# Kernel optimization log

Measured on AMD Instinct MI355X. Metric: run time of the kernel, lower is better.

## Reference

```python
import jax, jax.numpy as jnp
import numpy as np

B, D, V, T = 256, 1024, 32000, 64  # num_seqs, hidden dim, vocab, history len


def setup_inputs() -> dict:
    key = jax.random.key(0)
    ks = jax.random.split(key, 8)
    hidden = jax.random.normal(ks[0], (B, D), dtype=jnp.float32)
    embedding = jax.random.normal(ks[1], (V, D), dtype=jnp.float32) * (1.0 / np.sqrt(D))
    output_tokens = jax.random.randint(ks[2], (B, T), 0, V, dtype=jnp.int64)
    presence_penalties = jax.random.uniform(ks[3], (B,), dtype=jnp.float32)
    frequency_penalties = jax.random.uniform(ks[4], (B,), dtype=jnp.float32)
    temperatures = jax.random.uniform(ks[5], (B,), dtype=jnp.float32) + 0.5  # > eps
    top_ps = jax.random.uniform(ks[6], (B,), dtype=jnp.float32) * 0.5 + 0.5  # in [0.5, 1.0)
    top_ks = jax.random.randint(ks[7], (B,), 1, V, dtype=jnp.int64)
    return {
        "hidden": hidden,
        "embedding": embedding,
        "output_tokens": output_tokens,
        "presence_penalties": presence_penalties,
        "frequency_penalties": frequency_penalties,
        "temperatures": temperatures,
        "top_ps": top_ps,
        "top_ks": top_ks,
    }


def reference(hidden, embedding, output_tokens, presence_penalties,
              frequency_penalties, temperatures, top_ps, top_ks):
    # 1) logits = pruned hidden states @ embedding^T  -> [B, V]
    logits = jnp.einsum("bd,vd->bv", hidden, embedding)
    b, v = logits.shape

    # 2) presence/frequency penalties via per-row token histogram (np.bincount equiv)
    rows = jnp.broadcast_to(jnp.arange(b)[:, None], output_tokens.shape)
    counts = jnp.zeros((b, v), logits.dtype).at[rows, output_tokens].add(1.0)
    logits = logits - frequency_penalties[:, None] * counts \
                    - presence_penalties[:, None] * (counts > 0).astype(logits.dtype)

    # 3) temperature scaling
    logits = logits / temperatures[:, None]

    # 4) probabilities
    probs = jax.nn.softmax(logits, axis=-1)

    # 5) top-p / top-k: descending sort, cumsum masks, scatter back via inverse perm
    order = jnp.argsort(-probs, axis=-1)                       # descending order
    probs_sort = jnp.take_along_axis(probs, order, axis=-1)
    probs_cum = jnp.cumsum(probs_sort, axis=-1)
    top_p_mask = (probs_cum - probs_sort) > top_ps[:, None]
    top_k_mask = jnp.arange(v)[None, :] >= top_ks[:, None]
    probs_sort = jnp.where(top_p_mask | top_k_mask, 0.0, probs_sort)
    inv = jnp.argsort(order, axis=-1)
    filtered_probs = jnp.take_along_axis(probs_sort, inv, axis=-1)  # original order
    return filtered_probs
```

## Files before the change

### kernel.cpp

```cpp
#include <hip/hip_runtime.h>
#include <math.h>

#define NB 256
#define NV 32000
#define ND 1024
#define NT 64

#define GN 64
#define ASTR 40
#define NKB 64
#define ASLAB (256 * ASTR)
#define NGBLK (NV / GN)
#define INV2048F 4.8828125e-4f

#define NBIN 1024
#define HSTR 1032
#define HTOT (4 * HSTR)
#define FIX2 4294967296.0
#define SMASK ((1ull << 48) - 1ull)
#define SMEM_BYTES (NV * 4 + HTOT * 4)

typedef _Float16 f16x8 __attribute__((ext_vector_type(8)));
typedef _Float16 f16x4 __attribute__((ext_vector_type(4)));
typedef float f32x16 __attribute__((ext_vector_type(16)));
typedef __attribute__((address_space(3))) void lds_void;
typedef __attribute__((address_space(1))) void glb_void;

struct RowP2 {
  unsigned long long basePack;
  unsigned long long toppZfix;
  unsigned pfx;
  int ktop;
  float invZ;
  unsigned ustar;
  int m;
  int cEq;
};

__device__ __forceinline__ unsigned mono_enc(float f) {
  unsigned u = __float_as_uint(f);
  return (u & 0x80000000u) ? ~u : (u | 0x80000000u);
}
__device__ __forceinline__ float mono_dec(unsigned u) {
  return (u & 0x80000000u) ? __uint_as_float(u & 0x7FFFFFFFu) : __uint_as_float(~u);
}

__global__ __launch_bounds__(256) void convert_A(const float* __restrict__ hidden,
                                                 _Float16* __restrict__ A3) {
  const int g = blockIdx.x * 256 + threadIdx.x;
  const int kb = g >> 10, rc = g & 1023, r = rc >> 2, c = rc & 3;
  const float4 a4 = *(const float4*)(hidden + (size_t)r * ND + kb * 16 + c * 4);
  const float v[4] = {a4.x, a4.y, a4.z, a4.w};
  f16x4 h4, q4;
#pragma unroll
  for (int q = 0; q < 4; q++) {
    const _Float16 h = (_Float16)v[q];
    h4[q] = h;
    q4[q] = (_Float16)((v[q] - (float)h) * 2048.0f);
  }
  _Float16* base = A3 + (size_t)kb * ASLAB + r * ASTR;
  *(f16x4*)(base + c * 4) = h4;
  *(f16x4*)(base + 16 + c * 4) = q4;
}

__global__ __launch_bounds__(256, 2) void gemm_f16s(
    const float* __restrict__ Bm, const _Float16* __restrict__ A3,
    const float* __restrict__ temp, unsigned* __restrict__ rowmax,
    float* __restrict__ C) {
  __shared__ _Float16 Als[2][ASLAB];
  __shared__ _Float16 Bls[2][GN * ASTR];
  __shared__ float s_invT[256];
  __shared__ unsigned s_pm[256];

  const int t = threadIdx.x;
  const int l = t & 63, w = t >> 6;
  const int n0 = blockIdx.x * GN;
  s_invT[t] = 1.0f / temp[t];
  s_pm[t] = 0u;

  f32x16 accH[2][2] = {};
  f32x16 accC[2][2] = {};

  const int bn = t >> 2, bk4 = (t & 3) * 4;
  const int l31 = l & 31, lh = l >> 5;
  const int ka = lh * 8;
  const int mb = w * 64;

  const float* browp = Bm + (size_t)(n0 + bn) * ND + bk4;
  const char* gaBase = (const char*)A3 + w * 5120 + l * 16;
  char* laB0 = (char*)&Als[0][0] + w * 5120;
  char* laB1 = (char*)&Als[1][0] + w * 5120;

#define ISSUE_A(kbn, LA)                                                        \
  do {                                                                          \
    const char* ga_ = gaBase + (size_t)(kbn) * (ASLAB * 2);                     \
    _Pragma("unroll") for (int i_ = 0; i_ < 5; i_++)                            \
        __builtin_amdgcn_global_load_lds((const glb_void*)(ga_ + i_ * 1024),    \
                                         (lds_void*)((LA) + i_ * 1024), 16, 0,  \
                                         0);                                    \
  } while (0)

#define BCONV(BV, DST)                                                          \
  do {                                                                          \
    f16x4 h4_, q4_;                                                             \
    const float vv_[4] = {(BV).x, (BV).y, (BV).z, (BV).w};                      \
    _Pragma("unroll") for (int j_ = 0; j_ < 4; j_++) {                          \
      const _Float16 h_ = (_Float16)vv_[j_];                                    \
      h4_[j_] = h_;                                                             \
      q4_[j_] = (_Float16)((vv_[j_] - (float)h_) * 2048.0f);                    \
    }                                                                           \
    _Float16* prow_ = (DST) + bn * ASTR;                                        \
    *(f16x4*)(prow_ + bk4) = h4_;                                               \
    *(f16x4*)(prow_ + 16 + bk4) = q4_;                                          \
  } while (0)

#define COMPUTE(CUR)                                                                       \
  do {                                                                                     \
    const _Float16* Ap_ = &Als[CUR][0] + (size_t)(mb + l31) * ASTR + ka;                   \
    const _Float16* Bp_ = &Bls[CUR][0] + (size_t)l31 * ASTR + ka;                          \
    f16x8 a0h_ = *(const f16x8*)(Ap_);                                                     \
    f16x8 a1h_ = *(const f16x8*)(Ap_ + 32 * ASTR);                                         \
    f16x8 b0h_ = *(const f16x8*)(Bp_);                                                     \
    f16x8 b1h_ = *(const f16x8*)(Bp_ + 32 * ASTR);                                         \
    accH[0][0] = __builtin_amdgcn_mfma_f32_32x32x16_f16(a0h_, b0h_, accH[0][0], 0, 0, 0);  \
    accH[0][1] = __builtin_amdgcn_mfma_f32_32x32x16_f16(a0h_, b1h_, accH[0][1], 0, 0, 0);  \
    accH[1][0] = __builtin_amdgcn_mfma_f32_32x32x16_f16(a1h_, b0h_, accH[1][0], 0, 0, 0);  \
    accH[1][1] = __builtin_amdgcn_mfma_f32_32x32x16_f16(a1h_, b1h_, accH[1][1], 0, 0, 0);  \
    f16x8 b0q_ = *(const f16x8*)(Bp_ + 16);                                                \
    f16x8 b1q_ = *(const f16x8*)(Bp_ + 32 * ASTR + 16);                                    \
    accC[0][0] = __builtin_amdgcn_mfma_f32_32x32x16_f16(a0h_, b0q_, accC[0][0], 0, 0, 0);  \
    accC[0][1] = __builtin_amdgcn_mfma_f32_32x32x16_f16(a0h_, b1q_, accC[0][1], 0, 0, 0);  \
    accC[1][0] = __builtin_amdgcn_mfma_f32_32x32x16_f16(a1h_, b0q_, accC[1][0], 0, 0, 0);  \
    accC[1][1] = __builtin_amdgcn_mfma_f32_32x32x16_f16(a1h_, b1q_, accC[1][1], 0, 0, 0);  \
    f16x8 a0q_ = *(const f16x8*)(Ap_ + 16);                                                \
    f16x8 a1q_ = *(const f16x8*)(Ap_ + 32 * ASTR + 16);                                    \
    accC[0][0] = __builtin_amdgcn_mfma_f32_32x32x16_f16(a0q_, b0h_, accC[0][0], 0, 0, 0);  \
    accC[0][1] = __builtin_amdgcn_mfma_f32_32x32x16_f16(a0q_, b1h_, accC[0][1], 0, 0, 0);  \
    accC[1][0] = __builtin_amdgcn_mfma_f32_32x32x16_f16(a1q_, b0h_, accC[1][0], 0, 0, 0);  \
    accC[1][1] = __builtin_amdgcn_mfma_f32_32x32x16_f16(a1q_, b1h_, accC[1][1], 0, 0, 0);  \
  } while (0)

  ISSUE_A(0, laB0);
  __builtin_amdgcn_sched_barrier(0);
  float4 bv0 = *(const float4*)(browp);
  __builtin_amdgcn_sched_barrier(0);
  float4 bvA = *(const float4*)(browp + 16);
  __builtin_amdgcn_sched_barrier(0);
  asm volatile("s_waitcnt vmcnt(1)" ::: "memory");
  BCONV(bv0, &Bls[0][0]);
  asm volatile("s_waitcnt lgkmcnt(0)\ns_barrier" ::: "memory");

  float4 bvB;
  for (int kb = 0; kb < 62; kb += 2) {
    ISSUE_A(kb + 1, laB1);
    __builtin_amdgcn_sched_barrier(0);
    bvB = *(const float4*)(browp + (size_t)(kb + 2) * 16);
    __builtin_amdgcn_sched_barrier(0);
    asm volatile("s_waitcnt vmcnt(7)" ::: "memory");
    COMPUTE(0);
    __builtin_amdgcn_sched_barrier(0);
    asm volatile("s_waitcnt vmcnt(6)" ::: "memory");
    BCONV(bvA, &Bls[1][0]);
    asm volatile("s_waitcnt lgkmcnt(0)\ns_barrier" ::: "memory");

    ISSUE_A(kb + 2, laB0);
    __builtin_amdgcn_sched_barrier(0);
    bvA = *(const float4*)(browp + (size_t)(kb + 3) * 16);
    __builtin_amdgcn_sched_barrier(0);
    asm volatile("s_waitcnt vmcnt(7)" ::: "memory");
    COMPUTE(1);
    __builtin_amdgcn_sched_barrier(0);
    asm volatile("s_waitcnt vmcnt(6)" ::: "memory");
    BCONV(bvB, &Bls[0][0]);
    asm volatile("s_waitcnt lgkmcnt(0)\ns_barrier" ::: "memory");
  }

  ISSUE_A(63, laB1);
  __builtin_amdgcn_sched_barrier(0);
  asm volatile("s_waitcnt vmcnt(6)" ::: "memory");
  COMPUTE(0);
  __builtin_amdgcn_sched_barrier(0);
  asm volatile("s_waitcnt vmcnt(5)" ::: "memory");
  BCONV(bvA, &Bls[1][0]);
  asm volatile("s_waitcnt lgkmcnt(0)\ns_barrier" ::: "memory");

  asm volatile("s_waitcnt vmcnt(0)" ::: "memory");
  COMPUTE(1);

#undef ISSUE_A
#undef BCONV
#undef COMPUTE

#pragma unroll
  for (int mi = 0; mi < 2; mi++) {
#pragma unroll
    for (int r = 0; r < 16; r++) {
      const int row = mb + mi * 32 + (r & 3) + 8 * (r >> 2) + 4 * lh;
      const float it = s_invT[row];
      float v0 = (accH[mi][0][r] + accC[mi][0][r] * INV2048F) * it;
      float v1 = (accH[mi][1][r] + accC[mi][1][r] * INV2048F) * it;
      C[(size_t)row * NV + n0 + l31] = v0;
      C[(size_t)row * NV + n0 + 32 + l31] = v1;
      float mx = fmaxf(v0, v1);
#pragma unroll
      for (int o = 1; o < 32; o <<= 1) mx = fmaxf(mx, __shfl_xor(mx, o));
      if (l31 == 0) atomicMax(&s_pm[row], mono_enc(mx));
    }
  }
  __syncthreads();
  atomicMax(&rowmax[t], s_pm[t]);
}

__global__ __launch_bounds__(1024) void sample_row(
    float* __restrict__ buf, const unsigned* __restrict__ rowmax,
    const int* __restrict__ toks, const float* __restrict__ pres,
    const float* __restrict__ freq, const float* __restrict__ temp,
    const float* __restrict__ topp_a, const int* __restrict__ topk_a) {
  extern __shared__ char smem[];
  float* e = (float*)smem;
  unsigned* hist = (unsigned*)(smem + NV * 4);
  unsigned long long* suf = (unsigned long long*)hist;
  __shared__ int s_tok[NT];
  __shared__ int s_bs;
  __shared__ RowP2 sp;

  const int b = blockIdx.x, t = threadIdx.x;
  const int cp = (t >> 6) & 1;
  unsigned* loP = hist + cp * HSTR;
  unsigned* hcP = hist + 2 * HSTR + cp * HSTR;
  float* row = buf + (size_t)b * NV;

#define HACC(EV, BIN)                                                    \
  do {                                                                   \
    unsigned long long f_ = (unsigned long long)((double)(EV) * FIX2);   \
    unsigned flo_ = (unsigned)f_;                                        \
    unsigned old_ = atomicAdd(&loP[BIN], flo_);                          \
    unsigned hc_ = 0x10000u + (unsigned)(f_ >> 32) +                     \
                   ((old_ + flo_ < flo_) ? 1u : 0u);                     \
    atomicAdd(&hcP[BIN], hc_);                                           \
  } while (0)

  if (t < NT) s_tok[t] = toks[b * NT + t];
  for (int i = t; i < HTOT; i += 1024) hist[i] = 0u;
  for (int i4 = t; i4 < NV / 4; i4 += 1024)
    *(float4*)(e + i4 * 4) = *(const float4*)(row + i4 * 4);
  __syncthreads();

  if (t < NT) {
    const int tk = s_tok[t];
    bool first = true; int cnt = 0;
    for (int j = 0; j < NT; j++)
      if (s_tok[j] == tk) { if (j < t) first = false; cnt++; }
    if (first) e[tk] -= (freq[b] * (float)cnt + pres[b]) / temp[b];
  }
  __syncthreads();

  const float M = mono_dec(rowmax[b]);
  for (int i4 = t; i4 < NV / 4; i4 += 1024) {
    float4 x4 = *(const float4*)(e + i4 * 4);
    float4 e4;
    e4.x = expf(x4.x - M); e4.y = expf(x4.y - M);
    e4.z = expf(x4.z - M); e4.w = expf(x4.w - M);
    *(float4*)(e + i4 * 4) = e4;
    unsigned k;
    k = __float_as_uint(e4.x); if (k) HACC(e4.x, k >> 20);
    k = __float_as_uint(e4.y); if (k) HACC(e4.y, k >> 20);
    k = __float_as_uint(e4.z); if (k) HACC(e4.z, k >> 20);
    k = __float_as_uint(e4.w); if (k) HACC(e4.w, k >> 20);
  }
  __syncthreads();

  for (int level = 0; level < 3; level++) {
    const unsigned lo0 = hist[t], lo1 = hist[HSTR + t];
    const unsigned hc0 = hist[2 * HSTR + t], hc1 = hist[3 * HSTR + t];
    const unsigned c = (hc0 >> 16) + (hc1 >> 16);
    const unsigned long long sum =
        (((unsigned long long)((hc0 & 0xFFFFu) + (hc1 & 0xFFFFu))) << 32) +
        (unsigned long long)lo0 + (unsigned long long)lo1;
    const unsigned long long v = ((unsigned long long)c << 48) + sum;
    __syncthreads();
    suf[t] = v;
    __syncthreads();
    for (int off = 1; off < NBIN; off <<= 1) {
      unsigned long long add = (t + off < NBIN) ? suf[t + off] : 0ull;
      __syncthreads();
      suf[t] += add;
      __syncthreads();
    }
    const unsigned long long totalP = suf[0];
    if (t == 0) s_bs = NBIN - 1;
    __syncthreads();

    unsigned long long base, toppZ;
    int ktop_;
    if (level == 0) {
      ktop_ = topk_a[b];
      unsigned long long Zfix = totalP & SMASK;
      if (!Zfix) Zfix = 1ull;
      toppZ = (unsigned long long)((double)topp_a[b] * (double)Zfix);
      base = 0ull;
    } else {
      base = sp.basePack; toppZ = sp.toppZfix; ktop_ = sp.ktop;
    }

    {
      const unsigned long long sG = base + suf[t];
      const bool A = ((long long)(sG >> 48) < (long long)ktop_) && ((sG & SMASK) <= toppZ);
      const unsigned long long sP = base + ((t > 0) ? suf[t - 1] : totalP);
      const bool Ap = ((long long)(sP >> 48) < (long long)ktop_) && ((sP & SMASK) <= toppZ);
      if (A && !Ap) s_bs = t;
    }
    __syncthreads();
    if (t == 0) {
      const int bs = s_bs;
      const unsigned long long newBase = base + suf[bs];
      if (level == 0) {
        unsigned long long Zfix = totalP & SMASK;
        if (!Zfix) Zfix = 1ull;
        sp.invZ = (float)(FIX2 / (double)Zfix);
      }
      if (level < 2) {
        sp.basePack = newBase;
        sp.toppZfix = toppZ;
        sp.ktop = ktop_;
        sp.pfx = (level == 0) ? (unsigned)bs : ((sp.pfx << 10) | (unsigned)bs);
      } else {
        const unsigned ustar = (sp.pfx << 10) | (unsigned)bs;
        const unsigned long long raw = ((bs > 0) ? suf[bs - 1] : totalP) - suf[bs];
        const int cEq = (int)(raw >> 48);
        const long long Chi = (long long)(newBase >> 48);
        const unsigned long long Shi = newBase & SMASK;
        long long m = cEq;
        const long long lim = (long long)ktop_ - Chi;
        if (lim < m) m = lim;
        const double tf = (double)__uint_as_float(ustar) * FIX2;
        const double rem = (double)(toppZ - Shi);
        const double Rd = floor(rem / tf) + 1.0;
        if (Rd < (double)m) m = (long long)Rd;
        if (m < 1) m = 1;
        sp.ustar = ustar; sp.m = (int)m; sp.cEq = cEq;
      }
    }
    __syncthreads();

    if (level < 2) {
      for (int i = t; i < HTOT; i += 1024) hist[i] = 0u;
      __syncthreads();
      const unsigned pfx = sp.pfx;
      const int ms = (level == 0) ? 20 : 10;
      const int bsh = (level == 0) ? 10 : 0;
      for (int i4 = t; i4 < NV / 4; i4 += 1024) {
        float4 e4 = *(const float4*)(e + i4 * 4);
        unsigned k;
        k = __float_as_uint(e4.x); if (k && (k >> ms) == pfx) HACC(e4.x, (k >> bsh) & 1023u);
        k = __float_as_uint(e4.y); if (k && (k >> ms) == pfx) HACC(e4.y, (k >> bsh) & 1023u);
        k = __float_as_uint(e4.z); if (k && (k >> ms) == pfx) HACC(e4.z, (k >> bsh) & 1023u);
        k = __float_as_uint(e4.w); if (k && (k >> ms) == pfx) HACC(e4.w, (k >> bsh) & 1023u);
      }
      __syncthreads();
    }
  }
#undef HACC

  const unsigned ustar = sp.ustar;
  const float invZ = sp.invZ;
  if (sp.m >= sp.cEq) {
    for (int i4 = t; i4 < NV / 4; i4 += 1024) {
      float4 e4 = *(const float4*)(e + i4 * 4);
      float4 o4;
      unsigned k;
      k = __float_as_uint(e4.x); o4.x = (k >= ustar) ? e4.x * invZ : 0.f;
      k = __float_as_uint(e4.y); o4.y = (k >= ustar) ? e4.y * invZ : 0.f;
      k = __float_as_uint(e4.z); o4.z = (k >= ustar) ? e4.z * invZ : 0.f;
      k = __float_as_uint(e4.w); o4.w = (k >= ustar) ? e4.w * invZ : 0.f;
      *(float4*)(row + i4 * 4) = o4;
    }
  } else {
    const int m = sp.m;
    unsigned* rk = hist;
    const int base0 = t * 32;
    const int end0 = (base0 + 32 < NV) ? base0 + 32 : NV;
    int myc = 0;
    for (int v = base0; v < end0; v++)
      myc += (__float_as_uint(e[v]) == ustar);
    rk[t] = (unsigned)myc;
    __syncthreads();
    for (int off = 1; off < 1024; off <<= 1) {
      const unsigned a0 = rk[t];
      const unsigned an = (t >= off) ? rk[t - off] : 0u;
      __syncthreads();
      rk[t] = a0 + an;
      __syncthreads();
    }
    int r = (t > 0) ? (int)rk[t - 1] : 0;
    for (int v = base0; v < end0; v++) {
      const unsigned k = __float_as_uint(e[v]);
      float o = (k > ustar) ? e[v] * invZ : 0.f;
      if (k == ustar) { o = (r < m) ? e[v] * invZ : 0.f; r++; }
      row[v] = o;
    }
  }
}

extern "C" void kernel_launch(void* const* d_in, const int* in_sizes, int n_in,
                              void* d_out, int out_size, void* d_ws, size_t ws_size,
                              hipStream_t stream) {
  (void)in_sizes; (void)n_in; (void)out_size; (void)ws_size;
  const float* hidden = (const float*)d_in[0];
  const float* emb    = (const float*)d_in[1];
  const int*   toks   = (const int*)d_in[2];
  const float* pres   = (const float*)d_in[3];
  const float* freq   = (const float*)d_in[4];
  const float* temp   = (const float*)d_in[5];
  const float* topp   = (const float*)d_in[6];
  const int*   topk   = (const int*)d_in[7];
  float* out = (float*)d_out;

  const size_t offA3 = 0;
  const size_t offRM = 1310720;

  _Float16* A3 = (_Float16*)((char*)d_ws + offA3);
  unsigned* rowmax = (unsigned*)((char*)d_ws + offRM);

  hipFuncSetAttribute((const void*)sample_row,
                      hipFuncAttributeMaxDynamicSharedMemorySize, SMEM_BYTES);

  hipMemsetAsync((char*)d_ws + offRM, 0, 1024, stream);
  convert_A<<<256, 256, 0, stream>>>(hidden, A3);
  gemm_f16s<<<NGBLK, 256, 0, stream>>>(emb, A3, temp, rowmax, out);
  sample_row<<<NB, 1024, SMEM_BYTES, stream>>>(out, rowmax, toks, pres, freq,
                                               temp, topp, topk);
}
```

Baseline: 292.0 us.

## Split GEMM M dimension into two 128-row halves with grouped block order

The GEMM tile changes from 256 rows x 64 columns to 128 rows x 64 columns, giving 1000 active blocks instead of 500. Each wave now computes a 32x64 tile with fewer accumulators, and the launch bounds are raised to 4 blocks per CU. The hidden-state layout is rearranged into two halves per k-block, with a block index swizzle that pairs the two row halves of nearby column groups. This trades more parallelism and occupancy for reading each embedding tile twice, plus extra B conversion work.

```diff
diff --git a/kernel.cpp b/kernel.cpp
--- a/kernel.cpp
+++ b/kernel.cpp
@@ -7,10 +7,11 @@
 #define NT 64
 
 #define GN 64
+#define BM 128
 #define ASTR 40
 #define NKB 64
-#define ASLAB (256 * ASTR)
-#define NGBLK (NV / GN)
+#define AHALF 6144
+#define AKB (2 * AHALF)
 #define INV2048F 4.8828125e-4f
 
 #define NBIN 1024
@@ -49,52 +50,57 @@
                                                  _Float16* __restrict__ A3) {
   const int g = blockIdx.x * 256 + threadIdx.x;
   const int kb = g >> 10, rc = g & 1023, r = rc >> 2, c = rc & 3;
+  const int h = r >> 7, rr = r & 127;
   const float4 a4 = *(const float4*)(hidden + (size_t)r * ND + kb * 16 + c * 4);
   const float v[4] = {a4.x, a4.y, a4.z, a4.w};
   f16x4 h4, q4;
 #pragma unroll
   for (int q = 0; q < 4; q++) {
-    const _Float16 h = (_Float16)v[q];
-    h4[q] = h;
-    q4[q] = (_Float16)((v[q] - (float)h) * 2048.0f);
-  }
-  _Float16* base = A3 + (size_t)kb * ASLAB + r * ASTR;
+    const _Float16 hh = (_Float16)v[q];
+    h4[q] = hh;
+    q4[q] = (_Float16)((v[q] - (float)hh) * 2048.0f);
+  }
+  _Float16* base = A3 + (size_t)kb * AKB + h * AHALF + rr * ASTR;
   *(f16x4*)(base + c * 4) = h4;
   *(f16x4*)(base + 16 + c * 4) = q4;
 }
 
-__global__ __launch_bounds__(256, 2) void gemm_f16s(
+__global__ __launch_bounds__(256, 4) void gemm_f16s(
     const float* __restrict__ Bm, const _Float16* __restrict__ A3,
     const float* __restrict__ temp, unsigned* __restrict__ rowmax,
     float* __restrict__ C) {
-  __shared__ _Float16 Als[2][ASLAB];
+  __shared__ _Float16 Als[2][AHALF];
   __shared__ _Float16 Bls[2][GN * ASTR];
   __shared__ float s_invT[256];
   __shared__ unsigned s_pm[256];
 
+  const int bid = blockIdx.x;
+  const int x = bid & 7, h = (bid >> 3) & 1;
+  const int n = (bid >> 4) * 8 + x;
+  if (n >= NV / GN) return;
+  const int n0 = n * GN;
+
   const int t = threadIdx.x;
   const int l = t & 63, w = t >> 6;
-  const int n0 = blockIdx.x * GN;
   s_invT[t] = 1.0f / temp[t];
   s_pm[t] = 0u;
 
-  f32x16 accH[2][2] = {};
-  f32x16 accC[2][2] = {};
+  f32x16 accH[2] = {};
+  f32x16 accC[2] = {};
 
   const int bn = t >> 2, bk4 = (t & 3) * 4;
   const int l31 = l & 31, lh = l >> 5;
   const int ka = lh * 8;
-  const int mb = w * 64;
 
   const float* browp = Bm + (size_t)(n0 + bn) * ND + bk4;
-  const char* gaBase = (const char*)A3 + w * 5120 + l * 16;
-  char* laB0 = (char*)&Als[0][0] + w * 5120;
-  char* laB1 = (char*)&Als[1][0] + w * 5120;
+  const char* gaBase = (const char*)A3 + h * (AHALF * 2) + w * 3072 + l * 16;
+  char* laB0 = (char*)&Als[0][0] + w * 3072;
+  char* laB1 = (char*)&Als[1][0] + w * 3072;
 
 #define ISSUE_A(kbn, LA)                                                        \
   do {                                                                          \
-    const char* ga_ = gaBase + (size_t)(kbn) * (ASLAB * 2);                     \
-    _Pragma("unroll") for (int i_ = 0; i_ < 5; i_++)                            \
+    const char* ga_ = gaBase + (size_t)(kbn) * (AKB * 2);                       \
+    _Pragma("unroll") for (int i_ = 0; i_ < 3; i_++)                            \
         __builtin_amdgcn_global_load_lds((const glb_void*)(ga_ + i_ * 1024),    \
                                          (lds_void*)((LA) + i_ * 1024), 16, 0,  \
                                          0);                                    \
@@ -114,30 +120,22 @@
     *(f16x4*)(prow_ + 16 + bk4) = q4_;                                          \
   } while (0)
 
-#define COMPUTE(CUR)                                                                       \
-  do {                                                                                     \
-    const _Float16* Ap_ = &Als[CUR][0] + (size_t)(mb + l31) * ASTR + ka;                   \
-    const _Float16* Bp_ = &Bls[CUR][0] + (size_t)l31 * ASTR + ka;                          \
-    f16x8 a0h_ = *(const f16x8*)(Ap_);                                                     \
-    f16x8 a1h_ = *(const f16x8*)(Ap_ + 32 * ASTR);                                         \
-    f16x8 b0h_ = *(const f16x8*)(Bp_);                                                     \
-    f16x8 b1h_ = *(const f16x8*)(Bp_ + 32 * ASTR);                                         \
-    accH[0][0] = __builtin_amdgcn_mfma_f32_32x32x16_f16(a0h_, b0h_, accH[0][0], 0, 0, 0);  \
-    accH[0][1] = __builtin_amdgcn_mfma_f32_32x32x16_f16(a0h_, b1h_, accH[0][1], 0, 0, 0);  \
-    accH[1][0] = __builtin_amdgcn_mfma_f32_32x32x16_f16(a1h_, b0h_, accH[1][0], 0, 0, 0);  \
-    accH[1][1] = __builtin_amdgcn_mfma_f32_32x32x16_f16(a1h_, b1h_, accH[1][1], 0, 0, 0);  \
-    f16x8 b0q_ = *(const f16x8*)(Bp_ + 16);                                                \
-    f16x8 b1q_ = *(const f16x8*)(Bp_ + 32 * ASTR + 16);                                    \
-    accC[0][0] = __builtin_amdgcn_mfma_f32_32x32x16_f16(a0h_, b0q_, accC[0][0], 0, 0, 0);  \
-    accC[0][1] = __builtin_amdgcn_mfma_f32_32x32x16_f16(a0h_, b1q_, accC[0][1], 0, 0, 0);  \
-    accC[1][0] = __builtin_amdgcn_mfma_f32_32x32x16_f16(a1h_, b0q_, accC[1][0], 0, 0, 0);  \
-    accC[1][1] = __builtin_amdgcn_mfma_f32_32x32x16_f16(a1h_, b1q_, accC[1][1], 0, 0, 0);  \
-    f16x8 a0q_ = *(const f16x8*)(Ap_ + 16);                                                \
-    f16x8 a1q_ = *(const f16x8*)(Ap_ + 32 * ASTR + 16);                                    \
-    accC[0][0] = __builtin_amdgcn_mfma_f32_32x32x16_f16(a0q_, b0h_, accC[0][0], 0, 0, 0);  \
-    accC[0][1] = __builtin_amdgcn_mfma_f32_32x32x16_f16(a0q_, b1h_, accC[0][1], 0, 0, 0);  \
-    accC[1][0] = __builtin_amdgcn_mfma_f32_32x32x16_f16(a1q_, b0h_, accC[1][0], 0, 0, 0);  \
-    accC[1][1] = __builtin_amdgcn_mfma_f32_32x32x16_f16(a1q_, b1h_, accC[1][1], 0, 0, 0);  \
+#define COMPUTE(CUR)                                                                     \
+  do {                                                                                   \
+    const _Float16* Ap_ = &Als[CUR][0] + (size_t)(w * 32 + l31) * ASTR + ka;             \
+    const _Float16* Bp_ = &Bls[CUR][0] + (size_t)l31 * ASTR + ka;                        \
+    f16x8 ah_ = *(const f16x8*)(Ap_);                                                    \
+    f16x8 b0h_ = *(const f16x8*)(Bp_);                                                   \
+    f16x8 b1h_ = *(const f16x8*)(Bp_ + 32 * ASTR);                                       \
+    accH[0] = __builtin_amdgcn_mfma_f32_32x32x16_f16(ah_, b0h_, accH[0], 0, 0, 0);       \
+    accH[1] = __builtin_amdgcn_mfma_f32_32x32x16_f16(ah_, b1h_, accH[1], 0, 0, 0);       \
+    f16x8 b0q_ = *(const f16x8*)(Bp_ + 16);                                              \
+    f16x8 b1q_ = *(const f16x8*)(Bp_ + 32 * ASTR + 16);                                  \
+    accC[0] = __builtin_amdgcn_mfma_f32_32x32x16_f16(ah_, b0q_, accC[0], 0, 0, 0);       \
+    accC[1] = __builtin_amdgcn_mfma_f32_32x32x16_f16(ah_, b1q_, accC[1], 0, 0, 0);       \
+    f16x8 aq_ = *(const f16x8*)(Ap_ + 16);                                               \
+    accC[0] = __builtin_amdgcn_mfma_f32_32x32x16_f16(aq_, b0h_, accC[0], 0, 0, 0);       \
+    accC[1] = __builtin_amdgcn_mfma_f32_32x32x16_f16(aq_, b1h_, accC[1], 0, 0, 0);       \
   } while (0)
 
   ISSUE_A(0, laB0);
@@ -156,10 +154,10 @@
     __builtin_amdgcn_sched_barrier(0);
     bvB = *(const float4*)(browp + (size_t)(kb + 2) * 16);
     __builtin_amdgcn_sched_barrier(0);
-    asm volatile("s_waitcnt vmcnt(7)" ::: "memory");
+    asm volatile("s_waitcnt vmcnt(5)" ::: "memory");
     COMPUTE(0);
     __builtin_amdgcn_sched_barrier(0);
-    asm volatile("s_waitcnt vmcnt(6)" ::: "memory");
+    asm volatile("s_waitcnt vmcnt(4)" ::: "memory");
     BCONV(bvA, &Bls[1][0]);
     asm volatile("s_waitcnt lgkmcnt(0)\ns_barrier" ::: "memory");
 
@@ -167,20 +165,20 @@
     __builtin_amdgcn_sched_barrier(0);
     bvA = *(const float4*)(browp + (size_t)(kb + 3) * 16);
     __builtin_amdgcn_sched_barrier(0);
-    asm volatile("s_waitcnt vmcnt(7)" ::: "memory");
+    asm volatile("s_waitcnt vmcnt(5)" ::: "memory");
     COMPUTE(1);
     __builtin_amdgcn_sched_barrier(0);
-    asm volatile("s_waitcnt vmcnt(6)" ::: "memory");
+    asm volatile("s_waitcnt vmcnt(4)" ::: "memory");
     BCONV(bvB, &Bls[0][0]);
     asm volatile("s_waitcnt lgkmcnt(0)\ns_barrier" ::: "memory");
   }
 
   ISSUE_A(63, laB1);
   __builtin_amdgcn_sched_barrier(0);
-  asm volatile("s_waitcnt vmcnt(6)" ::: "memory");
+  asm volatile("s_waitcnt vmcnt(4)" ::: "memory");
   COMPUTE(0);
   __builtin_amdgcn_sched_barrier(0);
-  asm volatile("s_waitcnt vmcnt(5)" ::: "memory");
+  asm volatile("s_waitcnt vmcnt(3)" ::: "memory");
   BCONV(bvA, &Bls[1][0]);
   asm volatile("s_waitcnt lgkmcnt(0)\ns_barrier" ::: "memory");
 
@@ -192,20 +190,17 @@
 #undef COMPUTE
 
 #pragma unroll
-  for (int mi = 0; mi < 2; mi++) {
+  for (int r = 0; r < 16; r++) {
+    const int grow = h * BM + w * 32 + (r & 3) + 8 * (r >> 2) + 4 * lh;
+    const float it = s_invT[grow];
+    float v0 = (accH[0][r] + accC[0][r] * INV2048F) * it;
+    float v1 = (accH[1][r] + accC[1][r] * INV2048F) * it;
+    C[(size_t)grow * NV + n0 + l31] = v0;
+    C[(size_t)grow * NV + n0 + 32 + l31] = v1;
+    float mx = fmaxf(v0, v1);
 #pragma unroll
-    for (int r = 0; r < 16; r++) {
-      const int row = mb + mi * 32 + (r & 3) + 8 * (r >> 2) + 4 * lh;
-      const float it = s_invT[row];
-      float v0 = (accH[mi][0][r] + accC[mi][0][r] * INV2048F) * it;
-      float v1 = (accH[mi][1][r] + accC[mi][1][r] * INV2048F) * it;
-      C[(size_t)row * NV + n0 + l31] = v0;
-      C[(size_t)row * NV + n0 + 32 + l31] = v1;
-      float mx = fmaxf(v0, v1);
-#pragma unroll
-      for (int o = 1; o < 32; o <<= 1) mx = fmaxf(mx, __shfl_xor(mx, o));
-      if (l31 == 0) atomicMax(&s_pm[row], mono_enc(mx));
-    }
+    for (int o = 1; o < 32; o <<= 1) mx = fmaxf(mx, __shfl_xor(mx, o));
+    if (l31 == 0) atomicMax(&s_pm[grow], mono_enc(mx));
   }
   __syncthreads();
   atomicMax(&rowmax[t], s_pm[t]);
@@ -417,7 +412,7 @@
   float* out = (float*)d_out;
 
   const size_t offA3 = 0;
-  const size_t offRM = 1310720;
+  const size_t offRM = 1572864;
 
   _Float16* A3 = (_Float16*)((char*)d_ws + offA3);
   unsigned* rowmax = (unsigned*)((char*)d_ws + offRM);
@@ -427,7 +422,7 @@
 
   hipMemsetAsync((char*)d_ws + offRM, 0, 1024, stream);
   convert_A<<<256, 256, 0, stream>>>(hidden, A3);
-  gemm_f16s<<<NGBLK, 256, 0, stream>>>(emb, A3, temp, rowmax, out);
+  gemm_f16s<<<1008, 256, 0, stream>>>(emb, A3, temp, rowmax, out);
   sample_row<<<NB, 1024, SMEM_BYTES, stream>>>(out, rowmax, toks, pres, freq,
                                                temp, topp, topk);
 }
```

Result: slower. 303.5 us (+4.0%).

## Load pre-swizzled A fragments directly into registers instead of staging through LDS

Applied to the files above, without the earlier changes.

convert_A now writes the hidden-state f16 hi/lo split in the exact per-lane MFMA fragment order. The GEMM then loads the A operands straight from global memory into registers with a two-stage register double buffer, and drops the LDS A slabs along with the global_load_lds staging. This removes A traffic through LDS and the vmcnt waits that went with it, and frees shared memory. In exchange it relies on the compiler's implicit waits for the register loads, and adds VGPR pressure that may hurt occupancy under launch_bounds(256,2).

```diff
diff --git a/kernel.cpp b/kernel.cpp
--- a/kernel.cpp
+++ b/kernel.cpp
@@ -7,9 +7,9 @@
 #define NT 64
 
 #define GN 64
-#define ASTR 40
+#define BSTR 40
 #define NKB 64
-#define ASLAB (256 * ASTR)
+#define AKBF 8192
 #define NGBLK (NV / GN)
 #define INV2048F 4.8828125e-4f
 
@@ -23,8 +23,6 @@
 typedef _Float16 f16x8 __attribute__((ext_vector_type(8)));
 typedef _Float16 f16x4 __attribute__((ext_vector_type(4)));
 typedef float f32x16 __attribute__((ext_vector_type(16)));
-typedef __attribute__((address_space(3))) void lds_void;
-typedef __attribute__((address_space(1))) void glb_void;
 
 struct RowP2 {
   unsigned long long basePack;
@@ -48,27 +46,29 @@
 __global__ __launch_bounds__(256) void convert_A(const float* __restrict__ hidden,
                                                  _Float16* __restrict__ A3) {
   const int g = blockIdx.x * 256 + threadIdx.x;
-  const int kb = g >> 10, rc = g & 1023, r = rc >> 2, c = rc & 3;
+  const int kb = g >> 10, rem = g & 1023, r = rem >> 2, c = rem & 3;
   const float4 a4 = *(const float4*)(hidden + (size_t)r * ND + kb * 16 + c * 4);
   const float v[4] = {a4.x, a4.y, a4.z, a4.w};
   f16x4 h4, q4;
 #pragma unroll
   for (int q = 0; q < 4; q++) {
-    const _Float16 h = (_Float16)v[q];
-    h4[q] = h;
-    q4[q] = (_Float16)((v[q] - (float)h) * 2048.0f);
-  }
-  _Float16* base = A3 + (size_t)kb * ASLAB + r * ASTR;
-  *(f16x4*)(base + c * 4) = h4;
-  *(f16x4*)(base + 16 + c * 4) = q4;
+    const _Float16 hh = (_Float16)v[q];
+    h4[q] = hh;
+    q4[q] = (_Float16)((v[q] - (float)hh) * 2048.0f);
+  }
+  const int s = r >> 5, l31 = r & 31;
+  const int lh = c >> 1, j4 = (c & 1) * 4;
+  const int lane = l31 + (lh << 5);
+  _Float16* base = A3 + (size_t)kb * AKBF;
+  *(f16x4*)(base + ((s * 2 + 0) * 64 + lane) * 8 + j4) = h4;
+  *(f16x4*)(base + ((s * 2 + 1) * 64 + lane) * 8 + j4) = q4;
 }
 
 __global__ __launch_bounds__(256, 2) void gemm_f16s(
     const float* __restrict__ Bm, const _Float16* __restrict__ A3,
     const float* __restrict__ temp, unsigned* __restrict__ rowmax,
     float* __restrict__ C) {
-  __shared__ _Float16 Als[2][ASLAB];
-  __shared__ _Float16 Bls[2][GN * ASTR];
+  __shared__ _Float16 Bls[2][GN * BSTR];
   __shared__ float s_invT[256];
   __shared__ unsigned s_pm[256];
 
@@ -87,107 +87,93 @@
   const int mb = w * 64;
 
   const float* browp = Bm + (size_t)(n0 + bn) * ND + bk4;
-  const char* gaBase = (const char*)A3 + w * 5120 + l * 16;
-  char* laB0 = (char*)&Als[0][0] + w * 5120;
-  char* laB1 = (char*)&Als[1][0] + w * 5120;
-
-#define ISSUE_A(kbn, LA)                                                        \
-  do {                                                                          \
-    const char* ga_ = gaBase + (size_t)(kbn) * (ASLAB * 2);                     \
-    _Pragma("unroll") for (int i_ = 0; i_ < 5; i_++)                            \
-        __builtin_amdgcn_global_load_lds((const glb_void*)(ga_ + i_ * 1024),    \
-                                         (lds_void*)((LA) + i_ * 1024), 16, 0,  \
-                                         0);                                    \
+  const _Float16* aB = A3 + 2048 * w + l * 8;
+
+  f16x8 eh0, eh1, eq0, eq1;
+  f16x8 oh0, oh1, oq0, oq1;
+
+#define LOADA(P, KB)                                                  \
+  do {                                                                \
+    const _Float16* ap_ = aB + (size_t)(KB) * AKBF;                   \
+    P##h0 = *(const f16x8*)(ap_);                                     \
+    P##q0 = *(const f16x8*)(ap_ + 512);                               \
+    P##h1 = *(const f16x8*)(ap_ + 1024);                              \
+    P##q1 = *(const f16x8*)(ap_ + 1536);                              \
   } while (0)
 
-#define BCONV(BV, DST)                                                          \
-  do {                                                                          \
-    f16x4 h4_, q4_;                                                             \
-    const float vv_[4] = {(BV).x, (BV).y, (BV).z, (BV).w};                      \
-    _Pragma("unroll") for (int j_ = 0; j_ < 4; j_++) {                          \
-      const _Float16 h_ = (_Float16)vv_[j_];                                    \
-      h4_[j_] = h_;                                                             \
-      q4_[j_] = (_Float16)((vv_[j_] - (float)h_) * 2048.0f);                    \
-    }                                                                           \
-    _Float16* prow_ = (DST) + bn * ASTR;                                        \
-    *(f16x4*)(prow_ + bk4) = h4_;                                               \
-    *(f16x4*)(prow_ + 16 + bk4) = q4_;                                          \
+#define BCONV(BV, DST)                                                \
+  do {                                                                \
+    f16x4 h4_, q4_;                                                   \
+    const float vv_[4] = {(BV).x, (BV).y, (BV).z, (BV).w};            \
+    _Pragma("unroll") for (int j_ = 0; j_ < 4; j_++) {                \
+      const _Float16 h_ = (_Float16)vv_[j_];                          \
+      h4_[j_] = h_;                                                   \
+      q4_[j_] = (_Float16)((vv_[j_] - (float)h_) * 2048.0f);          \
+    }                                                                 \
+    _Float16* prow_ = (DST) + bn * BSTR;                              \
+    *(f16x4*)(prow_ + bk4) = h4_;                                     \
+    *(f16x4*)(prow_ + 16 + bk4) = q4_;                                \
   } while (0)
 
-#define COMPUTE(CUR)                                                                       \
-  do {                                                                                     \
-    const _Float16* Ap_ = &Als[CUR][0] + (size_t)(mb + l31) * ASTR + ka;                   \
-    const _Float16* Bp_ = &Bls[CUR][0] + (size_t)l31 * ASTR + ka;                          \
-    f16x8 a0h_ = *(const f16x8*)(Ap_);                                                     \
-    f16x8 a1h_ = *(const f16x8*)(Ap_ + 32 * ASTR);                                         \
-    f16x8 b0h_ = *(const f16x8*)(Bp_);                                                     \
-    f16x8 b1h_ = *(const f16x8*)(Bp_ + 32 * ASTR);                                         \
-    accH[0][0] = __builtin_amdgcn_mfma_f32_32x32x16_f16(a0h_, b0h_, accH[0][0], 0, 0, 0);  \
-    accH[0][1] = __builtin_amdgcn_mfma_f32_32x32x16_f16(a0h_, b1h_, accH[0][1], 0, 0, 0);  \
-    accH[1][0] = __builtin_amdgcn_mfma_f32_32x32x16_f16(a1h_, b0h_, accH[1][0], 0, 0, 0);  \
-    accH[1][1] = __builtin_amdgcn_mfma_f32_32x32x16_f16(a1h_, b1h_, accH[1][1], 0, 0, 0);  \
-    f16x8 b0q_ = *(const f16x8*)(Bp_ + 16);                                                \
-    f16x8 b1q_ = *(const f16x8*)(Bp_ + 32 * ASTR + 16);                                    \
-    accC[0][0] = __builtin_amdgcn_mfma_f32_32x32x16_f16(a0h_, b0q_, accC[0][0], 0, 0, 0);  \
-    accC[0][1] = __builtin_amdgcn_mfma_f32_32x32x16_f16(a0h_, b1q_, accC[0][1], 0, 0, 0);  \
-    accC[1][0] = __builtin_amdgcn_mfma_f32_32x32x16_f16(a1h_, b0q_, accC[1][0], 0, 0, 0);  \
-    accC[1][1] = __builtin_amdgcn_mfma_f32_32x32x16_f16(a1h_, b1q_, accC[1][1], 0, 0, 0);  \
-    f16x8 a0q_ = *(const f16x8*)(Ap_ + 16);                                                \
-    f16x8 a1q_ = *(const f16x8*)(Ap_ + 32 * ASTR + 16);                                    \
-    accC[0][0] = __builtin_amdgcn_mfma_f32_32x32x16_f16(a0q_, b0h_, accC[0][0], 0, 0, 0);  \
-    accC[0][1] = __builtin_amdgcn_mfma_f32_32x32x16_f16(a0q_, b1h_, accC[0][1], 0, 0, 0);  \
-    accC[1][0] = __builtin_amdgcn_mfma_f32_32x32x16_f16(a1q_, b0h_, accC[1][0], 0, 0, 0);  \
-    accC[1][1] = __builtin_amdgcn_mfma_f32_32x32x16_f16(a1q_, b1h_, accC[1][1], 0, 0, 0);  \
+#define COMPUTE(P, CUR)                                                                     \
+  do {                                                                                      \
+    const _Float16* Bp_ = &Bls[CUR][0] + (size_t)l31 * BSTR + ka;                           \
+    f16x8 b0h_ = *(const f16x8*)(Bp_);                                                      \
+    f16x8 b1h_ = *(const f16x8*)(Bp_ + 32 * BSTR);                                          \
+    accH[0][0] = __builtin_amdgcn_mfma_f32_32x32x16_f16(P##h0, b0h_, accH[0][0], 0, 0, 0);  \
+    accH[0][1] = __builtin_amdgcn_mfma_f32_32x32x16_f16(P##h0, b1h_, accH[0][1], 0, 0, 0);  \
+    accH[1][0] = __builtin_amdgcn_mfma_f32_32x32x16_f16(P##h1, b0h_, accH[1][0], 0, 0, 0);  \
+    accH[1][1] = __builtin_amdgcn_mfma_f32_32x32x16_f16(P##h1, b1h_, accH[1][1], 0, 0, 0);  \
+    f16x8 b0q_ = *(const f16x8*)(Bp_ + 16);                                                 \
+    f16x8 b1q_ = *(const f16x8*)(Bp_ + 32 * BSTR + 16);                                     \
+    accC[0][0] = __builtin_amdgcn_mfma_f32_32x32x16_f16(P##h0, b0q_, accC[0][0], 0, 0, 0);  \
+    accC[0][1] = __builtin_amdgcn_mfma_f32_32x32x16_f16(P##h0, b1q_, accC[0][1], 0, 0, 0);  \
+    accC[1][0] = __builtin_amdgcn_mfma_f32_32x32x16_f16(P##h1, b0q_, accC[1][0], 0, 0, 0);  \
+    accC[1][1] = __builtin_amdgcn_mfma_f32_32x32x16_f16(P##h1, b1q_, accC[1][1], 0, 0, 0);  \
+    accC[0][0] = __builtin_amdgcn_mfma_f32_32x32x16_f16(P##q0, b0h_, accC[0][0], 0, 0, 0);  \
+    accC[0][1] = __builtin_amdgcn_mfma_f32_32x32x16_f16(P##q0, b1h_, accC[0][1], 0, 0, 0);  \
+    accC[1][0] = __builtin_amdgcn_mfma_f32_32x32x16_f16(P##q1, b0h_, accC[1][0], 0, 0, 0);  \
+    accC[1][1] = __builtin_amdgcn_mfma_f32_32x32x16_f16(P##q1, b1h_, accC[1][1], 0, 0, 0);  \
   } while (0)
 
-  ISSUE_A(0, laB0);
+  LOADA(e, 0);
   __builtin_amdgcn_sched_barrier(0);
   float4 bv0 = *(const float4*)(browp);
   __builtin_amdgcn_sched_barrier(0);
+  LOADA(o, 1);
+  __builtin_amdgcn_sched_barrier(0);
   float4 bvA = *(const float4*)(browp + 16);
   __builtin_amdgcn_sched_barrier(0);
-  asm volatile("s_waitcnt vmcnt(1)" ::: "memory");
   BCONV(bv0, &Bls[0][0]);
   asm volatile("s_waitcnt lgkmcnt(0)\ns_barrier" ::: "memory");
 
   float4 bvB;
   for (int kb = 0; kb < 62; kb += 2) {
-    ISSUE_A(kb + 1, laB1);
+    COMPUTE(e, 0);
+    __builtin_amdgcn_sched_barrier(0);
+    LOADA(e, kb + 2);
     __builtin_amdgcn_sched_barrier(0);
     bvB = *(const float4*)(browp + (size_t)(kb + 2) * 16);
     __builtin_amdgcn_sched_barrier(0);
-    asm volatile("s_waitcnt vmcnt(7)" ::: "memory");
-    COMPUTE(0);
-    __builtin_amdgcn_sched_barrier(0);
-    asm volatile("s_waitcnt vmcnt(6)" ::: "memory");
     BCONV(bvA, &Bls[1][0]);
     asm volatile("s_waitcnt lgkmcnt(0)\ns_barrier" ::: "memory");
 
-    ISSUE_A(kb + 2, laB0);
+    COMPUTE(o, 1);
+    __builtin_amdgcn_sched_barrier(0);
+    LOADA(o, kb + 3);
     __builtin_amdgcn_sched_barrier(0);
     bvA = *(const float4*)(browp + (size_t)(kb + 3) * 16);
     __builtin_amdgcn_sched_barrier(0);
-    asm volatile("s_waitcnt vmcnt(7)" ::: "memory");
-    COMPUTE(1);
-    __builtin_amdgcn_sched_barrier(0);
-    asm volatile("s_waitcnt vmcnt(6)" ::: "memory");
     BCONV(bvB, &Bls[0][0]);
     asm volatile("s_waitcnt lgkmcnt(0)\ns_barrier" ::: "memory");
   }
-
-  ISSUE_A(63, laB1);
+  COMPUTE(e, 0);
   __builtin_amdgcn_sched_barrier(0);
-  asm volatile("s_waitcnt vmcnt(6)" ::: "memory");
-  COMPUTE(0);
-  __builtin_amdgcn_sched_barrier(0);
-  asm volatile("s_waitcnt vmcnt(5)" ::: "memory");
   BCONV(bvA, &Bls[1][0]);
   asm volatile("s_waitcnt lgkmcnt(0)\ns_barrier" ::: "memory");
-
-  asm volatile("s_waitcnt vmcnt(0)" ::: "memory");
-  COMPUTE(1);
-
-#undef ISSUE_A
+  COMPUTE(o, 1);
+
+#undef LOADA
 #undef BCONV
 #undef COMPUTE
 
@@ -417,7 +403,7 @@
   float* out = (float*)d_out;
 
   const size_t offA3 = 0;
-  const size_t offRM = 1310720;
+  const size_t offRM = 1048576;
 
   _Float16* A3 = (_Float16*)((char*)d_ws + offA3);
   unsigned* rowmax = (unsigned*)((char*)d_ws + offRM);
```

Measured after the change: 267.4 us. -8.4%, faster.
